# Performance work log

Hardware: AMD Instinct MI355X
Metric: run time of the kernel (lower is better)

The kernel has to match this reference:

```python
import jax, jax.numpy as jnp
import numpy as np

NT, NS, NH, NG, NR = 730, 2000, 16, 32, 15


def _lin_params(key, fan_in, fan_out):
    k1, k2 = jax.random.split(key)
    s = 1.0 / np.sqrt(fan_in)
    W = jax.random.uniform(k1, (fan_out, fan_in), minval=-s, maxval=s, dtype=jnp.float32)
    b = jax.random.uniform(k2, (fan_out,), minval=-s, maxval=s, dtype=jnp.float32)
    return W, b


def setup_inputs() -> dict:
    key = jax.random.key(0)
    ks = jax.random.split(key, 10)
    x = jax.random.normal(ks[0], (NT, NS, 6), dtype=jnp.float32)
    xc = jax.random.normal(ks[1], (NS, NG), dtype=jnp.float32)
    fc_W1, fc_b1 = _lin_params(ks[2], NG, 256)
    fc_W2, fc_b2 = _lin_params(ks[3], 256, NH * 10)
    fcR_W1, fcR_b1 = _lin_params(ks[4], NG, 256)
    fcR_W2, fcR_b2 = _lin_params(ks[5], 256, NH * NR)
    fcT1_W1, fcT1_b1 = _lin_params(ks[6], 1 + NG, 256)
    fcT1_W2, fcT1_b2 = _lin_params(ks[7], 256, NH * 2)
    fcT2_W1, fcT2_b1 = _lin_params(ks[8], 3 + NG, 256)
    fcT2_W2, fcT2_b2 = _lin_params(ks[9], 256, NH + 1)
    return dict(x=x, xc=xc,
                fc_W1=fc_W1, fc_b1=fc_b1, fc_W2=fc_W2, fc_b2=fc_b2,
                fcR_W1=fcR_W1, fcR_b1=fcR_b1, fcR_W2=fcR_W2, fcR_b2=fcR_b2,
                fcT1_W1=fcT1_W1, fcT1_b1=fcT1_b1, fcT1_W2=fcT1_W2, fcT1_b2=fcT1_b2,
                fcT2_W1=fcT2_W1, fcT2_b1=fcT2_b1, fcT2_W2=fcT2_W2, fcT2_b2=fcT2_b2)


def _mlp(z, W1, b1, W2, b2):
    # Linear -> Tanh -> Dropout(eval: identity) -> Linear
    h = jnp.tanh(z @ W1.T + b1)
    return h @ W2.T + b2


def _conv_ts(x, r):
    # causal per-(basin, bucket) temporal routing convolution
    # x: [nt, ns, nh], r: [ns, nh*nr] (relu'd routing weights)
    nt, ns, nh = x.shape
    nr = r.shape[-1] // nh
    xr = jnp.transpose(x, (1, 2, 0)).reshape(1, ns * nh, nt)   # [1, ns*nh, nt]
    k = r.reshape(ns * nh, 1, nr)
    y = jax.lax.conv_general_dilated(xr, k, (1,), [(nr - 1, 0)],
                                     feature_group_count=ns * nh)
    return jnp.transpose(y.reshape(ns, nh, nt), (2, 0, 1))     # [nt, ns, nh]


def _hsig(z):
    # F.hardsigmoid
    return jnp.clip(z / 6.0 + 0.5, 0.0, 1.0)


def _forward(x, xc, fc_W1, fc_b1, fc_W2, fc_b2, fcR_W1, fcR_b1, fcR_W2, fcR_b2,
             fcT1_W1, fcT1_b1, fcT1_W2, fcT1_b2, fcT2_W1, fcT2_b1, fcT2_W2, fcT2_b2):
    P, E, T1, T2, R, LAI = [x[:, :, i] for i in range(6)]
    nt, ns = P.shape
    nh = NH

    # snow/rain partition vp; masked positions get safe ratio to avoid nan grads
    mask = (T1 >= 0) | (T2 <= 0)
    denom = T2 - T1
    ratio = jnp.clip((T1 + T2) / jnp.where(denom == 0, 1.0, denom), -1.0, 1.0)
    ratio = jnp.where(mask, 0.0, ratio)
    vp = 1.0 - jnp.arccos(ratio) / 3.1415
    vp = jnp.where(T1 >= 0, 1.0, vp)
    vp = jnp.where(T2 <= 0, 0.0, vp)

    w = _mlp(xc, fc_W1, fc_b1, fc_W2, fc_b2)        # [ns, nh*10]
    wR = _mlp(xc, fcR_W1, fcR_b1, fcR_W2, fcR_b2)   # [ns, nh*nr]
    xc_t = jnp.broadcast_to(xc, (nt, ns, xc.shape[-1]))
    xcT1 = jnp.concatenate([LAI[:, :, None], xc_t], axis=-1)
    xcT2 = jnp.concatenate([R[:, :, None], T1[:, :, None], T2[:, :, None], xc_t], axis=-1)
    v1 = _mlp(xcT1, fcT1_W1, fcT1_b1, fcT1_W2, fcT1_b2)  # [nt, ns, nh*2]
    v2 = _mlp(xcT2, fcT2_W1, fcT2_b1, fcT2_W2, fcT2_b2)  # [nt, ns, nh+1]

    k1 = jax.nn.sigmoid(w[:, nh:2 * nh])
    k2 = jax.nn.sigmoid(w[:, 2 * nh:3 * nh])
    k23 = jax.nn.sigmoid(w[:, 3 * nh:4 * nh])
    k3 = jax.nn.sigmoid(w[:, 4 * nh:5 * nh]) / 10
    gl = jnp.exp(w[:, 5 * nh:6 * nh]) * 2
    ga = jax.nn.softmax(w[:, 6 * nh:7 * nh], axis=1)
    qb = jax.nn.relu(w[:, 7 * nh:8 * nh])
    ge1 = jax.nn.relu(w[:, 8 * nh:9 * nh])
    ge2 = jax.nn.relu(w[:, 9 * nh:10 * nh])

    vi = _hsig(v1[:, :, :nh])
    vk = _hsig(v1[:, :, nh:2 * nh])
    vm = jnp.exp(v2[:, :, :nh] * 2)

    Ps = P * (1 - vp)                     # [nt, ns]
    Pl = P * vp
    Pl1 = Pl[:, :, None] * (1 - vi)       # [nt, ns, nh]
    Pl2 = Pl[:, :, None] * vi
    Ev1 = E[:, :, None] * ge1
    Ev2 = E[:, :, None] * ge2

    def step(carry, inp):
        S0, Sv, S2, S3 = carry
        Ps_k, Pl1_k, Pl2_k, Ev1_k, Ev2_k, vk_k, vm_k = inp
        H0 = S0 + Ps_k[:, None]
        qSm = jnp.minimum(H0, vm_k)
        Hv = jax.nn.relu(Sv + Pl1_k - Ev1_k)
        qv = Sv * vk_k
        H2 = jax.nn.relu(S2 + qSm + qv - Ev2_k + Pl2_k)
        x1 = H2 - gl
        pos = x1 > 0
        Q1 = jnp.where(pos, jnp.power(jnp.where(pos, x1, 1.0), k1), 0.0)
        q2 = jnp.minimum(H2, gl) * k2
        Q2 = q2 * (1 - k23)
        H3 = S3 + q2 * k23
        Q3 = H3 * k3 + qb
        return (H0 - qSm, Hv - qv, H2 - Q1 - q2, H3 - Q3), (Q1, Q2, Q3)

    z = jnp.zeros((ns, nh), dtype=x.dtype)
    _, (Q1T, Q2T, Q3T) = jax.lax.scan(step, (z, z, z, z),
                                      (Ps, Pl1, Pl2, Ev1, Ev2, vk, vm))

    r = jax.nn.relu(wR)
    Q1R = _conv_ts(Q1T, r)
    Q2R = _conv_ts(Q2T, r)
    Q3R = _conv_ts(Q3T, r)
    return jnp.sum((Q1R + Q2R + Q3R) * ga, axis=2)   # [nt, ns]


def reference(x, xc, fc_W1, fc_b1, fc_W2, fc_b2, fcR_W1, fcR_b1, fcR_W2, fcR_b2,
              fcT1_W1, fcT1_b1, fcT1_W2, fcT1_b2, fcT2_W1, fcT2_b1, fcT2_W2, fcT2_b2):
    return _forward(x, xc, fc_W1, fc_b1, fc_W2, fc_b2, fcR_W1, fcR_b1, fcR_W2, fcR_b2,
                    fcT1_W1, fcT1_b1, fcT1_W2, fcT1_b2, fcT2_W1, fcT2_b1, fcT2_W2, fcT2_b2)
```

## Files before the change

### kernel.cpp

```cpp
#include <hip/hip_runtime.h>
#include <math.h>

#define NT 730
#define NS 2000
#define NH 16
#define NG 32
#define NR 15
#define HID 256
#define NSNH 32000

#define SC 2.885390081777927f
#define INV6 0.16666666666666666f

typedef _Float16 f16x8 __attribute__((ext_vector_type(8)));
typedef __fp16 fp16v2 __attribute__((ext_vector_type(2)));
typedef float f32x4 __attribute__((ext_vector_type(4)));

__device__ __forceinline__ float tanh_pre(float y) {
    float e = __builtin_amdgcn_exp2f(y);
    float r = __builtin_amdgcn_rcpf(e + 1.f);
    return fmaf(-2.f, r, 1.f);
}
__device__ __forceinline__ float fast_tanh(float x) { return tanh_pre(x * SC); }
__device__ __forceinline__ float sigmoidf_(float x) { return 1.f / (1.f + __expf(-x)); }

__device__ __forceinline__ f16x8 tanh8(float4 lo, float4 hi) {
    union { fp16v2 h[4]; f16x8 v; } u;
    u.h[0] = __builtin_amdgcn_cvt_pkrtz(tanh_pre(lo.x), tanh_pre(lo.y));
    u.h[1] = __builtin_amdgcn_cvt_pkrtz(tanh_pre(lo.z), tanh_pre(lo.w));
    u.h[2] = __builtin_amdgcn_cvt_pkrtz(tanh_pre(hi.x), tanh_pre(hi.y));
    u.h[3] = __builtin_amdgcn_cvt_pkrtz(tanh_pre(hi.z), tanh_pre(hi.w));
    return u.v;
}

__global__ __launch_bounds__(256) void k_pack(
    const float* __restrict__ T1W1, const float* __restrict__ T2W1,
    const float* __restrict__ T1W2, const float* __restrict__ T2W2,
    float4* __restrict__ CC4, _Float16* __restrict__ W2H)
{
    int k = threadIdx.x;
    CC4[k] = make_float4(SC * T1W1[k * (1 + NG)],
                         SC * T2W1[k * (3 + NG)],
                         SC * T2W1[k * (3 + NG) + 1],
                         SC * T2W1[k * (3 + NG) + 2]);
    for (int c = 0; c < 48; ++c) {
        float w = (c < 32) ? (INV6 * T1W2[c * HID + k]) : (SC * T2W2[(c - 32) * HID + k]);
        W2H[c * HID + k] = (_Float16)w;
    }
}

__global__ __launch_bounds__(256) void k_basin(
    const float* __restrict__ XC,
    const float* __restrict__ fcW1, const float* __restrict__ fcb1,
    const float* __restrict__ fcW2, const float* __restrict__ fcb2,
    const float* __restrict__ fRW1, const float* __restrict__ fRb1,
    const float* __restrict__ fRW2, const float* __restrict__ fRb2,
    const float* __restrict__ T1W1, const float* __restrict__ T1b1,
    const float* __restrict__ T2W1, const float* __restrict__ T2b1,
    float* __restrict__ P8, float* __restrict__ RKGA,
    float2* __restrict__ BASE12)
{
    const int s0 = blockIdx.x * 4, tid = threadIdx.x;
    __shared__ float xcs[4][NG];
    __shared__ float h[4][HID], hR[4][HID];
    __shared__ float wbuf[4][10 * NH], wRbuf[4][NH * NR];
    __shared__ float gav[4][NH];

    if (tid < 128) xcs[tid >> 5][tid & 31] = XC[(s0 + (tid >> 5)) * NG + (tid & 31)];
    __syncthreads();

    {
        float ab0 = fcb1[tid], ab1 = ab0, ab2 = ab0, ab3 = ab0;
        float rb0 = fRb1[tid], rb1 = rb0, rb2 = rb0, rb3 = rb0;
        const float4* w4  = (const float4*)(fcW1 + tid * NG);
        const float4* wR4 = (const float4*)(fRW1 + tid * NG);
#pragma unroll
        for (int g = 0; g < NG / 4; ++g) {
            float4 wv = w4[g], rv = wR4[g];
            float4 x0 = *(const float4*)&xcs[0][g * 4];
            float4 x1 = *(const float4*)&xcs[1][g * 4];
            float4 x2 = *(const float4*)&xcs[2][g * 4];
            float4 x3 = *(const float4*)&xcs[3][g * 4];
            ab0 += x0.x*wv.x + x0.y*wv.y + x0.z*wv.z + x0.w*wv.w;
            ab1 += x1.x*wv.x + x1.y*wv.y + x1.z*wv.z + x1.w*wv.w;
            ab2 += x2.x*wv.x + x2.y*wv.y + x2.z*wv.z + x2.w*wv.w;
            ab3 += x3.x*wv.x + x3.y*wv.y + x3.z*wv.z + x3.w*wv.w;
            rb0 += x0.x*rv.x + x0.y*rv.y + x0.z*rv.z + x0.w*rv.w;
            rb1 += x1.x*rv.x + x1.y*rv.y + x1.z*rv.z + x1.w*rv.w;
            rb2 += x2.x*rv.x + x2.y*rv.y + x2.z*rv.z + x2.w*rv.w;
            rb3 += x3.x*rv.x + x3.y*rv.y + x3.z*rv.z + x3.w*rv.w;
        }
        h[0][tid] = fast_tanh(ab0); h[1][tid] = fast_tanh(ab1);
        h[2][tid] = fast_tanh(ab2); h[3][tid] = fast_tanh(ab3);
        hR[0][tid] = fast_tanh(rb0); hR[1][tid] = fast_tanh(rb1);
        hR[2][tid] = fast_tanh(rb2); hR[3][tid] = fast_tanh(rb3);

        float b10 = T1b1[tid], b11 = b10, b12 = b10, b13 = b10;
        float b20 = T2b1[tid], b21 = b20, b22 = b20, b23 = b20;
        const float* w1 = T1W1 + tid * (1 + NG) + 1;
        const float* w2 = T2W1 + tid * (3 + NG) + 3;
#pragma unroll 8
        for (int g = 0; g < NG; ++g) {
            float w1g = w1[g], w2g = w2[g];
            float x0 = xcs[0][g], x1 = xcs[1][g], x2 = xcs[2][g], x3 = xcs[3][g];
            b10 = fmaf(x0, w1g, b10); b11 = fmaf(x1, w1g, b11);
            b12 = fmaf(x2, w1g, b12); b13 = fmaf(x3, w1g, b13);
            b20 = fmaf(x0, w2g, b20); b21 = fmaf(x1, w2g, b21);
            b22 = fmaf(x2, w2g, b22); b23 = fmaf(x3, w2g, b23);
        }
        BASE12[(size_t)(s0 + 0) * HID + tid] = make_float2(SC * b10, SC * b20);
        BASE12[(size_t)(s0 + 1) * HID + tid] = make_float2(SC * b11, SC * b21);
        BASE12[(size_t)(s0 + 2) * HID + tid] = make_float2(SC * b12, SC * b22);
        BASE12[(size_t)(s0 + 3) * HID + tid] = make_float2(SC * b13, SC * b23);
    }
    __syncthreads();

    if (tid < 10 * NH) {
        float a0 = fcb2[tid], a1 = a0, a2 = a0, a3 = a0;
        const float4* w4 = (const float4*)(fcW2 + tid * HID);
        for (int k = 0; k < HID / 4; ++k) {
            float4 wv = w4[k];
            float4 h0 = *(const float4*)&h[0][k * 4];
            float4 h1 = *(const float4*)&h[1][k * 4];
            float4 h2 = *(const float4*)&h[2][k * 4];
            float4 h3 = *(const float4*)&h[3][k * 4];
            a0 += h0.x*wv.x + h0.y*wv.y + h0.z*wv.z + h0.w*wv.w;
            a1 += h1.x*wv.x + h1.y*wv.y + h1.z*wv.z + h1.w*wv.w;
            a2 += h2.x*wv.x + h2.y*wv.y + h2.z*wv.z + h2.w*wv.w;
            a3 += h3.x*wv.x + h3.y*wv.y + h3.z*wv.z + h3.w*wv.w;
        }
        wbuf[0][tid] = a0; wbuf[1][tid] = a1; wbuf[2][tid] = a2; wbuf[3][tid] = a3;
    }
    if (tid < NH * NR) {
        float a0 = fRb2[tid], a1 = a0, a2 = a0, a3 = a0;
        const float4* w4 = (const float4*)(fRW2 + tid * HID);
        for (int k = 0; k < HID / 4; ++k) {
            float4 wv = w4[k];
            float4 h0 = *(const float4*)&hR[0][k * 4];
            float4 h1 = *(const float4*)&hR[1][k * 4];
            float4 h2 = *(const float4*)&hR[2][k * 4];
            float4 h3 = *(const float4*)&hR[3][k * 4];
            a0 += h0.x*wv.x + h0.y*wv.y + h0.z*wv.z + h0.w*wv.w;
            a1 += h1.x*wv.x + h1.y*wv.y + h1.z*wv.z + h1.w*wv.w;
            a2 += h2.x*wv.x + h2.y*wv.y + h2.z*wv.z + h2.w*wv.w;
            a3 += h3.x*wv.x + h3.y*wv.y + h3.z*wv.z + h3.w*wv.w;
        }
        wRbuf[0][tid] = a0; wRbuf[1][tid] = a1; wRbuf[2][tid] = a2; wRbuf[3][tid] = a3;
    }
    __syncthreads();

    if (tid < 64) {
        int b = tid >> 4, hh = tid & 15;
        const float* wb = wbuf[b];
        float mx = -1e30f;
        for (int i = 0; i < NH; ++i) mx = fmaxf(mx, wb[6 * NH + i]);
        float sum = 0.f;
        for (int i = 0; i < NH; ++i) sum += expf(wb[6 * NH + i] - mx);
        gav[b][hh] = expf(wb[6 * NH + hh] - mx) / sum;

        float* p = P8 + (size_t)((s0 + b) * NH + hh) * 8;
        p[0] = sigmoidf_(wb[1 * NH + hh]);
        p[1] = sigmoidf_(wb[2 * NH + hh]);
        p[2] = sigmoidf_(wb[3 * NH + hh]);
        p[3] = sigmoidf_(wb[4 * NH + hh]) * 0.1f;
        p[4] = expf(wb[5 * NH + hh]) * 2.f;
        p[5] = fmaxf(wb[7 * NH + hh], 0.f);
        p[6] = fmaxf(wb[8 * NH + hh], 0.f);
        p[7] = fmaxf(wb[9 * NH + hh], 0.f);
    }
    __syncthreads();

    for (int it = tid; it < 4 * NH * NR; it += 256) {
        int b = it / (NH * NR), r = it % (NH * NR);
        int hh = r / NR, j = r % NR;
        RKGA[(size_t)((s0 + b) * NH + hh) * 16 + (NR - 1 - j)] =
            gav[b][hh] * fmaxf(wRbuf[b][hh * NR + j], 0.f);
    }
}

__device__ __forceinline__ void store_pse(float4* __restrict__ PSE, long m, float2 pe, float2 t12) {
    float P = pe.x, E = pe.y, T1 = t12.x, T2 = t12.y;
    float den = T2 - T1;
    float ratio = (T1 + T2) / ((den == 0.f) ? 1.f : den);
    ratio = fminf(fmaxf(ratio, -1.f), 1.f);
    if ((T1 >= 0.f) || (T2 <= 0.f)) ratio = 0.f;
    float vp = 1.f - acosf(ratio) * (1.f / 3.1415f);
    if (T1 >= 0.f) vp = 1.f;
    if (T2 <= 0.f) vp = 0.f;
    PSE[m] = make_float4(P * (1.f - vp), P * vp, E, 0.f);
}

__global__ __launch_bounds__(64) void k_mlp(
    const float* __restrict__ X,
    const float2* __restrict__ BASE12, const float4* __restrict__ CC4,
    const _Float16* __restrict__ W2H,
    const float* __restrict__ T1b2, const float* __restrict__ T2b2,
    uint2* __restrict__ VMK, float4* __restrict__ PSE)
{
    const int lane = threadIdx.x;
    const int quad = lane >> 4, ml = lane & 15;
    const int s0 = blockIdx.x * 16;
    const int t0 = blockIdx.y * 4;
    const int srow = s0 + ml;

    const int tc0 = (t0 < NT) ? t0 : (NT - 1);
    const int tc1 = (t0 + 1 < NT) ? t0 + 1 : (NT - 1);
    const int tc2 = (t0 + 2 < NT) ? t0 + 2 : (NT - 1);
    const int tc3 = (t0 + 3 < NT) ? t0 + 3 : (NT - 1);

    const float* xr0 = X + ((long)tc0 * NS + srow) * 6;
    const float* xr1 = X + ((long)tc1 * NS + srow) * 6;
    const float* xr2 = X + ((long)tc2 * NS + srow) * 6;
    const float* xr3 = X + ((long)tc3 * NS + srow) * 6;
    float2 tt0 = *(const float2*)(xr0 + 2), rl0 = *(const float2*)(xr0 + 4);
    float2 tt1 = *(const float2*)(xr1 + 2), rl1 = *(const float2*)(xr1 + 4);
    float2 tt2 = *(const float2*)(xr2 + 2), rl2 = *(const float2*)(xr2 + 4);
    float2 tt3 = *(const float2*)(xr3 + 2), rl3 = *(const float2*)(xr3 + 4);

    const float bvi = fmaf(T1b2[ml], INV6, 0.5f);
    const float bvk = fmaf(T1b2[NH + ml], INV6, 0.5f);
    const float bvm = SC * T2b2[ml];
    f32x4 ac0_0 = {bvi, bvi, bvi, bvi}, ac0_1 = ac0_0, ac0_2 = ac0_0, ac0_3 = ac0_0;
    f32x4 ac1_0 = {bvk, bvk, bvk, bvk}, ac1_1 = ac1_0, ac1_2 = ac1_0, ac1_3 = ac1_0;
    f32x4 ac2_0 = {bvm, bvm, bvm, bvm}, ac2_1 = ac2_0, ac2_2 = ac2_0, ac2_3 = ac2_0;

    const float2* b12p = BASE12 + (size_t)srow * HID;
    const _Float16* wvi = W2H + (size_t)ml * HID;
    const _Float16* wvk = W2H + (size_t)(NH + ml) * HID;
    const _Float16* wvm = W2H + (size_t)(2 * NH + ml) * HID;

#pragma unroll 2
    for (int ks = 0; ks < 8; ++ks) {
        const int kb = ks * 32 + quad * 8;
        float4 cc0 = CC4[kb], cc1 = CC4[kb + 1], cc2 = CC4[kb + 2], cc3 = CC4[kb + 3];
        float4 cc4 = CC4[kb + 4], cc5 = CC4[kb + 5], cc6 = CC4[kb + 6], cc7 = CC4[kb + 7];
        float4 bA = *(const float4*)(b12p + kb);
        float4 bB = *(const float4*)(b12p + kb + 2);
        float4 bC = *(const float4*)(b12p + kb + 4);
        float4 bD = *(const float4*)(b12p + kb + 6);
        f16x8 Bvi = *(const f16x8*)(wvi + kb);
        f16x8 Bvk = *(const f16x8*)(wvk + kb);
        f16x8 Bvm = *(const f16x8*)(wvm + kb);

#define ARG2(CC, B2, TT, RL) fmaf(TT.y, CC.w, fmaf(TT.x, CC.z, fmaf(RL.x, CC.y, B2)))
#define DO_TILE(RL, TT, AC0, AC1, AC2) { \
        float4 a1lo = make_float4(fmaf(RL.y, cc0.x, bA.x), fmaf(RL.y, cc1.x, bA.z), \
                                  fmaf(RL.y, cc2.x, bB.x), fmaf(RL.y, cc3.x, bB.z)); \
        float4 a1hi = make_float4(fmaf(RL.y, cc4.x, bC.x), fmaf(RL.y, cc5.x, bC.z), \
                                  fmaf(RL.y, cc6.x, bD.x), fmaf(RL.y, cc7.x, bD.z)); \
        f16x8 Af1 = tanh8(a1lo, a1hi); \
        float4 a2lo = make_float4(ARG2(cc0, bA.y, TT, RL), ARG2(cc1, bA.w, TT, RL), \
                                  ARG2(cc2, bB.y, TT, RL), ARG2(cc3, bB.w, TT, RL)); \
        float4 a2hi = make_float4(ARG2(cc4, bC.y, TT, RL), ARG2(cc5, bC.w, TT, RL), \
                                  ARG2(cc6, bD.y, TT, RL), ARG2(cc7, bD.w, TT, RL)); \
        f16x8 Af2 = tanh8(a2lo, a2hi); \
        AC0 = __builtin_amdgcn_mfma_f32_16x16x32_f16(Af1, Bvi, AC0, 0, 0, 0); \
        AC1 = __builtin_amdgcn_mfma_f32_16x16x32_f16(Af1, Bvk, AC1, 0, 0, 0); \
        AC2 = __builtin_amdgcn_mfma_f32_16x16x32_f16(Af2, Bvm, AC2, 0, 0, 0); }

        DO_TILE(rl0, tt0, ac0_0, ac1_0, ac2_0)
        DO_TILE(rl1, tt1, ac0_1, ac1_1, ac2_1)
        DO_TILE(rl2, tt2, ac0_2, ac1_2, ac2_2)
        DO_TILE(rl3, tt3, ac0_3, ac1_3, ac2_3)
#undef DO_TILE
#undef ARG2
    }

#define EPI(TC, AC0, AC1, AC2) { \
    long rowbase = (long)TC * NS + s0 + quad * 4; \
    _Pragma("unroll") \
    for (int rg = 0; rg < 4; ++rg) { \
        float vi = fminf(fmaxf(AC0[rg], 0.f), 1.f); \
        float vk = fminf(fmaxf(AC1[rg], 0.f), 1.f); \
        float vm = __builtin_amdgcn_exp2f(AC2[rg]); \
        unsigned pk = (unsigned)(vi * 65535.f + 0.5f) | ((unsigned)(vk * 65535.f + 0.5f) << 16); \
        VMK[(rowbase + rg) * NH + ml] = make_uint2(pk, __float_as_uint(vm)); \
    } }

    EPI(tc0, ac0_0, ac1_0, ac2_0)
    EPI(tc1, ac0_1, ac1_1, ac2_1)
    EPI(tc2, ac0_2, ac1_2, ac2_2)
    EPI(tc3, ac0_3, ac1_3, ac2_3)
#undef EPI

    {
        int tq = t0 + quad; if (tq >= NT) tq = NT - 1;
        const float* xq = X + ((long)tq * NS + srow) * 6;
        float2 peq = *(const float2*)xq;
        float2 ttq = *(const float2*)(xq + 2);
        store_pse(PSE, (long)tq * NS + srow, peq, ttq);
    }
}

__global__ __launch_bounds__(64) void k_scan(
    const uint2* __restrict__ VMK, const float4* __restrict__ PSE,
    const float* __restrict__ P8, const float* __restrict__ RKGA,
    _Float16* __restrict__ YH)
{
    int lane = threadIdx.x;
    int s = blockIdx.x * 4 + (lane >> 4);
    int hh = lane & 15;
    size_t ch = (size_t)s * NH + hh;

    const float4* pp = (const float4*)(P8 + (size_t)ch * 8);
    float4 pa = pp[0], pb4 = pp[1];
    float k1 = pa.x, k2 = pa.y, k23 = pa.z, k3 = pa.w;
    float gl = pb4.x, qb = pb4.y, ge1 = pb4.z, ge2 = pb4.w;

    float rk[16];
    {
        const float4* rp = (const float4*)(RKGA + (size_t)ch * 16);
#pragma unroll
        for (int i = 0; i < 4; ++i) {
            float4 v = rp[i];
            rk[4 * i] = v.x; rk[4 * i + 1] = v.y; rk[4 * i + 2] = v.z; rk[4 * i + 3] = v.w;
        }
    }

    float S0 = 0.f, Sv = 0.f, S2 = 0.f, S3 = 0.f;
    float qr[14];
#pragma unroll
    for (int i = 0; i < 14; ++i) qr[i] = 0.f;

    uint2 vb[14]; float4 pbf[14];
#pragma unroll
    for (int i = 0; i < 14; ++i) {
        vb[i] = VMK[(size_t)i * NSNH + ch];
        pbf[i] = PSE[(size_t)i * NS + s];
    }

    int t = 0;
#define SBODY(I) { \
    uint2 v = vb[I]; float4 ps = pbf[I]; \
    int t2 = t + 14; if (t2 > NT - 1) t2 = NT - 1; \
    vb[I] = VMK[(size_t)t2 * NSNH + ch]; \
    pbf[I] = PSE[(size_t)t2 * NS + s]; \
    float vi = (float)(v.x & 0xffffu) * (1.f / 65535.f); \
    float vk = (float)(v.x >> 16) * (1.f / 65535.f); \
    float vm = __uint_as_float(v.y); \
    float Ps = ps.x, Pl = ps.y, E = ps.z; \
    float H0 = S0 + Ps; \
    float qSm = fminf(H0, vm); S0 = H0 - qSm; \
    float Hv = fmaxf(Sv + Pl * (1.f - vi) - E * ge1, 0.f); \
    float qv = Sv * vk; Sv = Hv - qv; \
    float H2 = fmaxf(S2 + qSm + qv - E * ge2 + Pl * vi, 0.f); \
    float x1 = H2 - gl; \
    float Q1 = (x1 > 0.f) ? __expf(k1 * __logf(x1)) : 0.f; \
    float q2 = fminf(H2, gl) * k2; \
    float Q2 = q2 * (1.f - k23); \
    float H3 = S3 + q2 * k23; \
    float Q3 = H3 * k3 + qb; \
    S2 = H2 - Q1 - q2; S3 = H3 - Q3; \
    float qt = Q1 + Q2 + Q3; \
    float y = qt * rk[0]; \
    _Pragma("unroll") for (int d = 1; d <= 14; ++d) y += qr[((I) + 14 - d) % 14] * rk[d]; \
    qr[I] = qt; \
    YH[(size_t)t * NSNH + ch] = (_Float16)y; \
    ++t; }

    for (int tb = 0; tb < 52; ++tb) {
        SBODY(0) SBODY(1) SBODY(2) SBODY(3) SBODY(4) SBODY(5) SBODY(6)
        SBODY(7) SBODY(8) SBODY(9) SBODY(10) SBODY(11) SBODY(12) SBODY(13)
    }
    SBODY(0) SBODY(1)
#undef SBODY
}

__global__ __launch_bounds__(256) void k_reduce(
    const _Float16* __restrict__ YH, float* __restrict__ OUT)
{
    long m = (long)blockIdx.x * 256 + threadIdx.x;
    if (m >= (long)NT * NS) return;
    int t = (int)(m / NS), s = (int)(m % NS);
    const _Float16* q = YH + (size_t)t * NSNH + (size_t)s * NH;
    f16x8 a = *(const f16x8*)q;
    f16x8 b = *(const f16x8*)(q + 8);
    float acc = 0.f;
#pragma unroll
    for (int i = 0; i < 8; ++i) acc += (float)a[i];
#pragma unroll
    for (int i = 0; i < 8; ++i) acc += (float)b[i];
    OUT[m] = acc;
}

extern "C" void kernel_launch(void* const* d_in, const int* in_sizes, int n_in,
                              void* d_out, int out_size, void* d_ws, size_t ws_size,
                              hipStream_t stream)
{
    const float* X    = (const float*)d_in[0];
    const float* XC   = (const float*)d_in[1];
    const float* fcW1 = (const float*)d_in[2];
    const float* fcb1 = (const float*)d_in[3];
    const float* fcW2 = (const float*)d_in[4];
    const float* fcb2 = (const float*)d_in[5];
    const float* fRW1 = (const float*)d_in[6];
    const float* fRb1 = (const float*)d_in[7];
    const float* fRW2 = (const float*)d_in[8];
    const float* fRb2 = (const float*)d_in[9];
    const float* T1W1 = (const float*)d_in[10];
    const float* T1b1 = (const float*)d_in[11];
    const float* T1W2 = (const float*)d_in[12];
    const float* T1b2 = (const float*)d_in[13];
    const float* T2W1 = (const float*)d_in[14];
    const float* T2b1 = (const float*)d_in[15];
    const float* T2W2 = (const float*)d_in[16];
    const float* T2b2 = (const float*)d_in[17];
    float* OUT = (float*)d_out;

    char* w = (char*)d_ws;
    uint2* VMK     = (uint2*)w;     w += (size_t)NT * NSNH * 8;
    float4* PSE    = (float4*)w;    w += (size_t)NT * NS * 16;
    _Float16* YH   = (_Float16*)w;  w += (size_t)NT * NSNH * 2;
    float2* BASE12 = (float2*)w;    w += (size_t)NS * HID * 8;
    float* P8      = (float*)w;     w += (size_t)NS * NH * 8 * 4;
    float* RKGA    = (float*)w;     w += (size_t)NS * NH * 16 * 4;
    _Float16* W2H  = (_Float16*)w;  w += 48 * HID * 2;
    float4* CC4    = (float4*)w;    w += HID * 16;
    (void)ws_size; (void)in_sizes; (void)n_in; (void)out_size;

    k_pack<<<dim3(1), dim3(256), 0, stream>>>(T1W1, T2W1, T1W2, T2W2, CC4, W2H);
    k_basin<<<dim3(NS / 4), dim3(256), 0, stream>>>(XC, fcW1, fcb1, fcW2, fcb2,
                                                    fRW1, fRb1, fRW2, fRb2,
                                                    T1W1, T1b1, T2W1, T2b1,
                                                    P8, RKGA, BASE12);
    k_mlp<<<dim3(125, 183), dim3(64), 0, stream>>>(
        X, BASE12, CC4, W2H, T1b2, T2b2, VMK, PSE);
    k_scan<<<dim3(NS / 4), dim3(64), 0, stream>>>(VMK, PSE, P8, RKGA, YH);
    k_reduce<<<dim3((unsigned)(((long)NT * NS + 255) / 256)), dim3(256), 0, stream>>>(YH, OUT);
}
```

Measured before the change: 547.8 us.

## Fuse MLP producer and scan consumer into one kernel with per-chunk atomic flags

```diff
diff --git a/kernel.cpp b/kernel.cpp
--- a/kernel.cpp
+++ b/kernel.cpp
@@ -8,6 +8,8 @@
 #define NR 15
 #define HID 256
 #define NSNH 32000
+#define NCHUNK 183
+#define PROD_PER_CHUNK 125
 
 #define SC 2.885390081777927f
 #define INV6 0.16666666666666666f
@@ -15,6 +17,7 @@
 typedef _Float16 f16x8 __attribute__((ext_vector_type(8)));
 typedef __fp16 fp16v2 __attribute__((ext_vector_type(2)));
 typedef float f32x4 __attribute__((ext_vector_type(4)));
+typedef unsigned u32x2 __attribute__((ext_vector_type(2)));
 
 __device__ __forceinline__ float tanh_pre(float y) {
     float e = __builtin_amdgcn_exp2f(y);
@@ -33,10 +36,17 @@
     return u.v;
 }
 
+__device__ __forceinline__ void wait_chunk(int* done, int c) {
+    while (__hip_atomic_load(&done[c], __ATOMIC_RELAXED, __HIP_MEMORY_SCOPE_AGENT)
+           < PROD_PER_CHUNK)
+        __builtin_amdgcn_s_sleep(4);
+    (void)__hip_atomic_load(&done[c], __ATOMIC_ACQUIRE, __HIP_MEMORY_SCOPE_WORKGROUP);
+}
+
 __global__ __launch_bounds__(256) void k_pack(
     const float* __restrict__ T1W1, const float* __restrict__ T2W1,
     const float* __restrict__ T1W2, const float* __restrict__ T2W2,
-    float4* __restrict__ CC4, _Float16* __restrict__ W2H)
+    float4* __restrict__ CC4, _Float16* __restrict__ W2H, int* __restrict__ done)
 {
     int k = threadIdx.x;
     CC4[k] = make_float4(SC * T1W1[k * (1 + NG)],
@@ -47,6 +57,7 @@
         float w = (c < 32) ? (INV6 * T1W2[c * HID + k]) : (SC * T2W2[(c - 32) * HID + k]);
         W2H[c * HID + k] = (_Float16)w;
     }
+    if (k < NCHUNK + 1) done[k] = 0;
 }
 
 __global__ __launch_bounds__(256) void k_basin(
@@ -178,126 +189,130 @@
     }
 }
 
-__device__ __forceinline__ void store_pse(float4* __restrict__ PSE, long m, float2 pe, float2 t12) {
-    float P = pe.x, E = pe.y, T1 = t12.x, T2 = t12.y;
-    float den = T2 - T1;
-    float ratio = (T1 + T2) / ((den == 0.f) ? 1.f : den);
-    ratio = fminf(fmaxf(ratio, -1.f), 1.f);
-    if ((T1 >= 0.f) || (T2 <= 0.f)) ratio = 0.f;
-    float vp = 1.f - acosf(ratio) * (1.f / 3.1415f);
-    if (T1 >= 0.f) vp = 1.f;
-    if (T2 <= 0.f) vp = 0.f;
-    PSE[m] = make_float4(P * (1.f - vp), P * vp, E, 0.f);
-}
-
-__global__ __launch_bounds__(64) void k_mlp(
+__global__ __launch_bounds__(64) void k_fused(
     const float* __restrict__ X,
     const float2* __restrict__ BASE12, const float4* __restrict__ CC4,
     const _Float16* __restrict__ W2H,
     const float* __restrict__ T1b2, const float* __restrict__ T2b2,
-    uint2* __restrict__ VMK, float4* __restrict__ PSE)
+    const float* __restrict__ P8, const float* __restrict__ RKGA,
+    uint2* __restrict__ VMK, float4* __restrict__ PSE,
+    _Float16* __restrict__ YH, int* __restrict__ done)
 {
     const int lane = threadIdx.x;
-    const int quad = lane >> 4, ml = lane & 15;
-    const int s0 = blockIdx.x * 16;
-    const int t0 = blockIdx.y * 4;
-    const int srow = s0 + ml;
-
-    const int tc0 = (t0 < NT) ? t0 : (NT - 1);
-    const int tc1 = (t0 + 1 < NT) ? t0 + 1 : (NT - 1);
-    const int tc2 = (t0 + 2 < NT) ? t0 + 2 : (NT - 1);
-    const int tc3 = (t0 + 3 < NT) ? t0 + 3 : (NT - 1);
-
-    const float* xr0 = X + ((long)tc0 * NS + srow) * 6;
-    const float* xr1 = X + ((long)tc1 * NS + srow) * 6;
-    const float* xr2 = X + ((long)tc2 * NS + srow) * 6;
-    const float* xr3 = X + ((long)tc3 * NS + srow) * 6;
-    float2 tt0 = *(const float2*)(xr0 + 2), rl0 = *(const float2*)(xr0 + 4);
-    float2 tt1 = *(const float2*)(xr1 + 2), rl1 = *(const float2*)(xr1 + 4);
-    float2 tt2 = *(const float2*)(xr2 + 2), rl2 = *(const float2*)(xr2 + 4);
-    float2 tt3 = *(const float2*)(xr3 + 2), rl3 = *(const float2*)(xr3 + 4);
-
-    const float bvi = fmaf(T1b2[ml], INV6, 0.5f);
-    const float bvk = fmaf(T1b2[NH + ml], INV6, 0.5f);
-    const float bvm = SC * T2b2[ml];
-    f32x4 ac0_0 = {bvi, bvi, bvi, bvi}, ac0_1 = ac0_0, ac0_2 = ac0_0, ac0_3 = ac0_0;
-    f32x4 ac1_0 = {bvk, bvk, bvk, bvk}, ac1_1 = ac1_0, ac1_2 = ac1_0, ac1_3 = ac1_0;
-    f32x4 ac2_0 = {bvm, bvm, bvm, bvm}, ac2_1 = ac2_0, ac2_2 = ac2_0, ac2_3 = ac2_0;
-
-    const float2* b12p = BASE12 + (size_t)srow * HID;
-    const _Float16* wvi = W2H + (size_t)ml * HID;
-    const _Float16* wvk = W2H + (size_t)(NH + ml) * HID;
-    const _Float16* wvm = W2H + (size_t)(2 * NH + ml) * HID;
+
+    if (blockIdx.x >= 500) {
+        const int p = blockIdx.x - 500;
+        const int tchunk = p / PROD_PER_CHUNK;
+        const int sblk = p % PROD_PER_CHUNK;
+        const int quad = lane >> 4, ml = lane & 15;
+        const int s0 = sblk * 16;
+        const int t0 = tchunk * 4;
+        const int srow = s0 + ml;
+
+        const int tc0 = (t0 < NT) ? t0 : (NT - 1);
+        const int tc1 = (t0 + 1 < NT) ? t0 + 1 : (NT - 1);
+        const int tc2 = (t0 + 2 < NT) ? t0 + 2 : (NT - 1);
+        const int tc3 = (t0 + 3 < NT) ? t0 + 3 : (NT - 1);
+
+        const float* xr0 = X + ((long)tc0 * NS + srow) * 6;
+        const float* xr1 = X + ((long)tc1 * NS + srow) * 6;
+        const float* xr2 = X + ((long)tc2 * NS + srow) * 6;
+        const float* xr3 = X + ((long)tc3 * NS + srow) * 6;
+        float2 tt0 = *(const float2*)(xr0 + 2), rl0 = *(const float2*)(xr0 + 4);
+        float2 tt1 = *(const float2*)(xr1 + 2), rl1 = *(const float2*)(xr1 + 4);
+        float2 tt2 = *(const float2*)(xr2 + 2), rl2 = *(const float2*)(xr2 + 4);
+        float2 tt3 = *(const float2*)(xr3 + 2), rl3 = *(const float2*)(xr3 + 4);
+
+        const float bvi = fmaf(T1b2[ml], INV6, 0.5f);
+        const float bvk = fmaf(T1b2[NH + ml], INV6, 0.5f);
+        const float bvm = SC * T2b2[ml];
+        f32x4 ac0_0 = {bvi, bvi, bvi, bvi}, ac0_1 = ac0_0, ac0_2 = ac0_0, ac0_3 = ac0_0;
+        f32x4 ac1_0 = {bvk, bvk, bvk, bvk}, ac1_1 = ac1_0, ac1_2 = ac1_0, ac1_3 = ac1_0;
+        f32x4 ac2_0 = {bvm, bvm, bvm, bvm}, ac2_1 = ac2_0, ac2_2 = ac2_0, ac2_3 = ac2_0;
+
+        const float2* b12p = BASE12 + (size_t)srow * HID;
+        const _Float16* wvi = W2H + (size_t)ml * HID;
+        const _Float16* wvk = W2H + (size_t)(NH + ml) * HID;
+        const _Float16* wvm = W2H + (size_t)(2 * NH + ml) * HID;
 
 #pragma unroll 2
-    for (int ks = 0; ks < 8; ++ks) {
-        const int kb = ks * 32 + quad * 8;
-        float4 cc0 = CC4[kb], cc1 = CC4[kb + 1], cc2 = CC4[kb + 2], cc3 = CC4[kb + 3];
-        float4 cc4 = CC4[kb + 4], cc5 = CC4[kb + 5], cc6 = CC4[kb + 6], cc7 = CC4[kb + 7];
-        float4 bA = *(const float4*)(b12p + kb);
-        float4 bB = *(const float4*)(b12p + kb + 2);
-        float4 bC = *(const float4*)(b12p + kb + 4);
-        float4 bD = *(const float4*)(b12p + kb + 6);
-        f16x8 Bvi = *(const f16x8*)(wvi + kb);
-        f16x8 Bvk = *(const f16x8*)(wvk + kb);
-        f16x8 Bvm = *(const f16x8*)(wvm + kb);
+        for (int ks = 0; ks < 8; ++ks) {
+            const int kb = ks * 32 + quad * 8;
+            float4 cc0 = CC4[kb], cc1 = CC4[kb + 1], cc2 = CC4[kb + 2], cc3 = CC4[kb + 3];
+            float4 cc4 = CC4[kb + 4], cc5 = CC4[kb + 5], cc6 = CC4[kb + 6], cc7 = CC4[kb + 7];
+            float4 bA = *(const float4*)(b12p + kb);
+            float4 bB = *(const float4*)(b12p + kb + 2);
+            float4 bC = *(const float4*)(b12p + kb + 4);
+            float4 bD = *(const float4*)(b12p + kb + 6);
+            f16x8 Bvi = *(const f16x8*)(wvi + kb);
+            f16x8 Bvk = *(const f16x8*)(wvk + kb);
+            f16x8 Bvm = *(const f16x8*)(wvm + kb);
 
 #define ARG2(CC, B2, TT, RL) fmaf(TT.y, CC.w, fmaf(TT.x, CC.z, fmaf(RL.x, CC.y, B2)))
 #define DO_TILE(RL, TT, AC0, AC1, AC2) { \
-        float4 a1lo = make_float4(fmaf(RL.y, cc0.x, bA.x), fmaf(RL.y, cc1.x, bA.z), \
-                                  fmaf(RL.y, cc2.x, bB.x), fmaf(RL.y, cc3.x, bB.z)); \
-        float4 a1hi = make_float4(fmaf(RL.y, cc4.x, bC.x), fmaf(RL.y, cc5.x, bC.z), \
-                                  fmaf(RL.y, cc6.x, bD.x), fmaf(RL.y, cc7.x, bD.z)); \
-        f16x8 Af1 = tanh8(a1lo, a1hi); \
-        float4 a2lo = make_float4(ARG2(cc0, bA.y, TT, RL), ARG2(cc1, bA.w, TT, RL), \
-                                  ARG2(cc2, bB.y, TT, RL), ARG2(cc3, bB.w, TT, RL)); \
-        float4 a2hi = make_float4(ARG2(cc4, bC.y, TT, RL), ARG2(cc5, bC.w, TT, RL), \
-                                  ARG2(cc6, bD.y, TT, RL), ARG2(cc7, bD.w, TT, RL)); \
-        f16x8 Af2 = tanh8(a2lo, a2hi); \
-        AC0 = __builtin_amdgcn_mfma_f32_16x16x32_f16(Af1, Bvi, AC0, 0, 0, 0); \
-        AC1 = __builtin_amdgcn_mfma_f32_16x16x32_f16(Af1, Bvk, AC1, 0, 0, 0); \
-        AC2 = __builtin_amdgcn_mfma_f32_16x16x32_f16(Af2, Bvm, AC2, 0, 0, 0); }
-
-        DO_TILE(rl0, tt0, ac0_0, ac1_0, ac2_0)
-        DO_TILE(rl1, tt1, ac0_1, ac1_1, ac2_1)
-        DO_TILE(rl2, tt2, ac0_2, ac1_2, ac2_2)
-        DO_TILE(rl3, tt3, ac0_3, ac1_3, ac2_3)
+            float4 a1lo = make_float4(fmaf(RL.y, cc0.x, bA.x), fmaf(RL.y, cc1.x, bA.z), \
+                                      fmaf(RL.y, cc2.x, bB.x), fmaf(RL.y, cc3.x, bB.z)); \
+            float4 a1hi = make_float4(fmaf(RL.y, cc4.x, bC.x), fmaf(RL.y, cc5.x, bC.z), \
+                                      fmaf(RL.y, cc6.x, bD.x), fmaf(RL.y, cc7.x, bD.z)); \
+            f16x8 Af1 = tanh8(a1lo, a1hi); \
+            float4 a2lo = make_float4(ARG2(cc0, bA.y, TT, RL), ARG2(cc1, bA.w, TT, RL), \
+                                      ARG2(cc2, bB.y, TT, RL), ARG2(cc3, bB.w, TT, RL)); \
+            float4 a2hi = make_float4(ARG2(cc4, bC.y, TT, RL), ARG2(cc5, bC.w, TT, RL), \
+                                      ARG2(cc6, bD.y, TT, RL), ARG2(cc7, bD.w, TT, RL)); \
+            f16x8 Af2 = tanh8(a2lo, a2hi); \
+            AC0 = __builtin_amdgcn_mfma_f32_16x16x32_f16(Af1, Bvi, AC0, 0, 0, 0); \
+            AC1 = __builtin_amdgcn_mfma_f32_16x16x32_f16(Af1, Bvk, AC1, 0, 0, 0); \
+            AC2 = __builtin_amdgcn_mfma_f32_16x16x32_f16(Af2, Bvm, AC2, 0, 0, 0); }
+
+            DO_TILE(rl0, tt0, ac0_0, ac1_0, ac2_0)
+            DO_TILE(rl1, tt1, ac0_1, ac1_1, ac2_1)
+            DO_TILE(rl2, tt2, ac0_2, ac1_2, ac2_2)
+            DO_TILE(rl3, tt3, ac0_3, ac1_3, ac2_3)
 #undef DO_TILE
 #undef ARG2
-    }
+        }
 
 #define EPI(TC, AC0, AC1, AC2) { \
-    long rowbase = (long)TC * NS + s0 + quad * 4; \
-    _Pragma("unroll") \
-    for (int rg = 0; rg < 4; ++rg) { \
-        float vi = fminf(fmaxf(AC0[rg], 0.f), 1.f); \
-        float vk = fminf(fmaxf(AC1[rg], 0.f), 1.f); \
-        float vm = __builtin_amdgcn_exp2f(AC2[rg]); \
-        unsigned pk = (unsigned)(vi * 65535.f + 0.5f) | ((unsigned)(vk * 65535.f + 0.5f) << 16); \
-        VMK[(rowbase + rg) * NH + ml] = make_uint2(pk, __float_as_uint(vm)); \
-    } }
-
-    EPI(tc0, ac0_0, ac1_0, ac2_0)
-    EPI(tc1, ac0_1, ac1_1, ac2_1)
-    EPI(tc2, ac0_2, ac1_2, ac2_2)
-    EPI(tc3, ac0_3, ac1_3, ac2_3)
+        long rowbase = (long)TC * NS + s0 + quad * 4; \
+        _Pragma("unroll") \
+        for (int rg = 0; rg < 4; ++rg) { \
+            float vi = fminf(fmaxf(AC0[rg], 0.f), 1.f); \
+            float vk = fminf(fmaxf(AC1[rg], 0.f), 1.f); \
+            float vm = __builtin_amdgcn_exp2f(AC2[rg]); \
+            unsigned pk = (unsigned)(vi * 65535.f + 0.5f) | ((unsigned)(vk * 65535.f + 0.5f) << 16); \
+            u32x2 pv; pv.x = pk; pv.y = __float_as_uint(vm); \
+            __builtin_nontemporal_store(pv, (u32x2*)&VMK[(rowbase + rg) * NH + ml]); \
+        } }
+
+        EPI(tc0, ac0_0, ac1_0, ac2_0)
+        EPI(tc1, ac0_1, ac1_1, ac2_1)
+        EPI(tc2, ac0_2, ac1_2, ac2_2)
+        EPI(tc3, ac0_3, ac1_3, ac2_3)
 #undef EPI
 
-    {
-        int tq = t0 + quad; if (tq >= NT) tq = NT - 1;
-        const float* xq = X + ((long)tq * NS + srow) * 6;
-        float2 peq = *(const float2*)xq;
-        float2 ttq = *(const float2*)(xq + 2);
-        store_pse(PSE, (long)tq * NS + srow, peq, ttq);
-    }
-}
-
-__global__ __launch_bounds__(64) void k_scan(
-    const uint2* __restrict__ VMK, const float4* __restrict__ PSE,
-    const float* __restrict__ P8, const float* __restrict__ RKGA,
-    _Float16* __restrict__ YH)
-{
-    int lane = threadIdx.x;
+        {
+            int tq = t0 + quad; if (tq >= NT) tq = NT - 1;
+            const float* xq = X + ((long)tq * NS + srow) * 6;
+            float2 pe = *(const float2*)xq;
+            float2 tt = *(const float2*)(xq + 2);
+            float P = pe.x, E = pe.y, T1 = tt.x, T2 = tt.y;
+            float den = T2 - T1;
+            float ratio = (T1 + T2) / ((den == 0.f) ? 1.f : den);
+            ratio = fminf(fmaxf(ratio, -1.f), 1.f);
+            if ((T1 >= 0.f) || (T2 <= 0.f)) ratio = 0.f;
+            float vp = 1.f - acosf(ratio) * (1.f / 3.1415f);
+            if (T1 >= 0.f) vp = 1.f;
+            if (T2 <= 0.f) vp = 0.f;
+            f32x4 psv; psv[0] = P * (1.f - vp); psv[1] = P * vp; psv[2] = E; psv[3] = 0.f;
+            __builtin_nontemporal_store(psv, (f32x4*)&PSE[(long)tq * NS + srow]);
+        }
+
+        if (lane == 0)
+            __hip_atomic_fetch_add(&done[tchunk], 1, __ATOMIC_RELEASE,
+                                   __HIP_MEMORY_SCOPE_AGENT);
+        return;
+    }
+
     int s = blockIdx.x * 4 + (lane >> 4);
     int hh = lane & 15;
     size_t ch = (size_t)s * NH + hh;
@@ -318,23 +333,27 @@
     }
 
     float S0 = 0.f, Sv = 0.f, S2 = 0.f, S3 = 0.f;
-    float qr[14];
-#pragma unroll
-    for (int i = 0; i < 14; ++i) qr[i] = 0.f;
-
-    uint2 vb[14]; float4 pbf[14];
-#pragma unroll
-    for (int i = 0; i < 14; ++i) {
+    float qr[16];
+#pragma unroll
+    for (int i = 0; i < 16; ++i) qr[i] = 0.f;
+
+    uint2 vb[4]; float4 pbf[4];
+    wait_chunk(done, 0);
+#pragma unroll
+    for (int i = 0; i < 4; ++i) {
         vb[i] = VMK[(size_t)i * NSNH + ch];
         pbf[i] = PSE[(size_t)i * NS + s];
     }
 
     int t = 0;
 #define SBODY(I) { \
-    uint2 v = vb[I]; float4 ps = pbf[I]; \
-    int t2 = t + 14; if (t2 > NT - 1) t2 = NT - 1; \
-    vb[I] = VMK[(size_t)t2 * NSNH + ch]; \
-    pbf[I] = PSE[(size_t)t2 * NS + s]; \
+    uint2 v = vb[(I) & 3]; float4 ps = pbf[(I) & 3]; \
+    int t2 = t + 4; \
+    if (t2 <= NT - 1) { \
+        if (((I) & 3) == 0) wait_chunk(done, t2 >> 2); \
+        vb[(I) & 3] = VMK[(size_t)t2 * NSNH + ch]; \
+        pbf[(I) & 3] = PSE[(size_t)t2 * NS + s]; \
+    } \
     float vi = (float)(v.x & 0xffffu) * (1.f / 65535.f); \
     float vk = (float)(v.x >> 16) * (1.f / 65535.f); \
     float vm = __uint_as_float(v.y); \
@@ -353,16 +372,17 @@
     S2 = H2 - Q1 - q2; S3 = H3 - Q3; \
     float qt = Q1 + Q2 + Q3; \
     float y = qt * rk[0]; \
-    _Pragma("unroll") for (int d = 1; d <= 14; ++d) y += qr[((I) + 14 - d) % 14] * rk[d]; \
+    _Pragma("unroll") for (int d = 1; d <= 14; ++d) y += qr[((I) + 16 - d) & 15] * rk[d]; \
     qr[I] = qt; \
     YH[(size_t)t * NSNH + ch] = (_Float16)y; \
     ++t; }
 
-    for (int tb = 0; tb < 52; ++tb) {
-        SBODY(0) SBODY(1) SBODY(2) SBODY(3) SBODY(4) SBODY(5) SBODY(6)
-        SBODY(7) SBODY(8) SBODY(9) SBODY(10) SBODY(11) SBODY(12) SBODY(13)
-    }
-    SBODY(0) SBODY(1)
+    for (int tb = 0; tb < 45; ++tb) {
+        SBODY(0) SBODY(1) SBODY(2) SBODY(3) SBODY(4) SBODY(5) SBODY(6) SBODY(7)
+        SBODY(8) SBODY(9) SBODY(10) SBODY(11) SBODY(12) SBODY(13) SBODY(14) SBODY(15)
+    }
+    SBODY(0) SBODY(1) SBODY(2) SBODY(3) SBODY(4)
+    SBODY(5) SBODY(6) SBODY(7) SBODY(8) SBODY(9)
 #undef SBODY
 }
 
@@ -416,15 +436,15 @@
     float* RKGA    = (float*)w;     w += (size_t)NS * NH * 16 * 4;
     _Float16* W2H  = (_Float16*)w;  w += 48 * HID * 2;
     float4* CC4    = (float4*)w;    w += HID * 16;
+    int* DONE      = (int*)w;       w += (NCHUNK + 1) * 4;
     (void)ws_size; (void)in_sizes; (void)n_in; (void)out_size;
 
-    k_pack<<<dim3(1), dim3(256), 0, stream>>>(T1W1, T2W1, T1W2, T2W2, CC4, W2H);
+    k_pack<<<dim3(1), dim3(256), 0, stream>>>(T1W1, T2W1, T1W2, T2W2, CC4, W2H, DONE);
     k_basin<<<dim3(NS / 4), dim3(256), 0, stream>>>(XC, fcW1, fcb1, fcW2, fcb2,
                                                     fRW1, fRb1, fRW2, fRb2,
                                                     T1W1, T1b1, T2W1, T2b1,
                                                     P8, RKGA, BASE12);
-    k_mlp<<<dim3(125, 183), dim3(64), 0, stream>>>(
-        X, BASE12, CC4, W2H, T1b2, T2b2, VMK, PSE);
-    k_scan<<<dim3(NS / 4), dim3(64), 0, stream>>>(VMK, PSE, P8, RKGA, YH);
+    k_fused<<<dim3(500 + NCHUNK * PROD_PER_CHUNK), dim3(64), 0, stream>>>(
+        X, BASE12, CC4, W2H, T1b2, T2b2, P8, RKGA, VMK, PSE, YH, DONE);
     k_reduce<<<dim3((unsigned)(((long)NT * NS + 255) / 256)), dim3(256), 0, stream>>>(YH, OUT);
 }
```

New measurement: 1.544 ms. +181.9%, slower.
